# Kernel tuning notes

Hardware: AMD Instinct MI355X
Metric: run time of the kernel (lower is better)

The kernel has to match this reference:

```python
import jax, jax.numpy as jnp
import numpy as np


def setup_inputs() -> dict:
    key = jax.random.key(0)
    ks = jax.random.split(key, 7)
    T, D, V = 2048, 1024, 28  # frames, encoder hidden, vocab_size
    s = 0.05  # keras 'random_normal' initializer stddev
    return {
        "x": jax.random.normal(ks[0], (1, T, D), jnp.float32),
        "Wa": jax.random.normal(ks[1], (1, V), jnp.float32) * s,
        "Ua": jax.random.normal(ks[2], (1, D), jnp.float32) * s,
        "Va": jax.random.normal(ks[3], (1, 1), jnp.float32) * s,
        "Wo": jax.random.normal(ks[4], (V, V), jnp.float32) * s,
        "Uo": jax.random.normal(ks[5], (V, D), jnp.float32) * s,
        "Co": jax.random.normal(ks[6], (V, D), jnp.float32) * s,
    }


def reference(x, Wa, Ua, Va, Wo, Uo, Co):
    # Source uses only the first batch element: x = x[0]
    xb = x[0]                      # (T, D)
    V = Wo.shape[0]
    D = Uo.shape[1]
    # Ua . x[j] is constant across outer steps t (source recomputes it; math identical)
    ux = xb @ Ua[0]                # (T,)

    def step(carry, xt):
        Y, H = carry               # Y: (V,) previous output, H: (D,) previous frame
        prev = Wa[0] @ Y           # scalar: Wa . Yanterior
        scores = Va[0, 0] * jnp.tanh(ux + prev)   # (T,)
        # Source applies K.softmax (axis=-1) to scores of shape (T,1,1):
        # softmax over a size-1 axis -> all ones. Reproduced faithfully.
        w = jax.nn.softmax(scores[:, None], axis=-1)   # (T, 1), all ones
        context = (xb * w).sum(axis=0)                 # (D,)
        y = jax.nn.sigmoid(Wo @ Y + Uo @ H + Co @ context)  # (V,)
        return (y, xt), y          # Hanterior <- x[t]

    init = (jnp.zeros((V,), xb.dtype), jnp.zeros((D,), xb.dtype))
    _, ys = jax.lax.scan(step, init, xb)   # ys: (T, V)
    return ys[None]                        # (1, T, V)
```

## Files before the change

### kernel.cpp

```cpp
#include <hip/hip_runtime.h>

#define T_FRAMES 2048
#define D_DIM    1024
#define V_DIM    28
#define BSTRIDE  32
#define CSTRIDE  32
#define LOG2E_F  1.44269504088896f

#define CHUNK    8
#define WARM     24
#define NCHUNK   (T_FRAMES / CHUNK)

#define RPB      4
#define NB_PREP  (T_FRAMES / RPB)

__global__ __launch_bounds__(256) void prep_kernel(const float* __restrict__ x,
                                                   const float* __restrict__ Uo,
                                                   const float* __restrict__ Co,
                                                   float* __restrict__ cpart,
                                                   float* __restrict__ Bmat) {
    int tid = threadIdx.x, b = blockIdx.x;
    __shared__ float xs[RPB * D_DIM];
    __shared__ float cs[D_DIM];

    int wave = tid >> 6, lane = tid & 63;

    const float4* xb4 = (const float4*)(x + (size_t)b * RPB * D_DIM);
    float4 xv0 = xb4[0 * (D_DIM / 4) + tid];
    float4 xv1 = xb4[1 * (D_DIM / 4) + tid];
    float4 xv2 = xb4[2 * (D_DIM / 4) + tid];
    float4 xv3 = xb4[3 * (D_DIM / 4) + tid];

    float4 u[7][4];
#pragma unroll
    for (int q = 0; q < 7; ++q) {
        const float4* u4 = (const float4*)(Uo + (size_t)(wave * 7 + q) * D_DIM);
#pragma unroll
        for (int m = 0; m < 4; ++m) u[q][m] = u4[lane + 64 * m];
    }

    ((float4*)xs)[0 * (D_DIM / 4) + tid] = xv0;
    ((float4*)xs)[1 * (D_DIM / 4) + tid] = xv1;
    ((float4*)xs)[2 * (D_DIM / 4) + tid] = xv2;
    ((float4*)xs)[3 * (D_DIM / 4) + tid] = xv3;
    float4 csum;
    csum.x = (xv0.x + xv1.x) + (xv2.x + xv3.x);
    csum.y = (xv0.y + xv1.y) + (xv2.y + xv3.y);
    csum.z = (xv0.z + xv1.z) + (xv2.z + xv3.z);
    csum.w = (xv0.w + xv1.w) + (xv2.w + xv3.w);
    ((float4*)cs)[tid] = csum;
    __syncthreads();

#pragma unroll
    for (int q = 0; q < 7; ++q) {
        int i = wave * 7 + q;
        const float4* c4 = (const float4*)(Co + (size_t)i * D_DIM);
        float acc = 0.f;
#pragma unroll
        for (int m = 0; m < 4; ++m) {
            float4 a = c4[lane + 64 * m];
            float4 d = ((const float4*)cs)[lane + 64 * m];
            acc += a.x * d.x + a.y * d.y + a.z * d.z + a.w * d.w;
        }
#pragma unroll
        for (int off = 32; off > 0; off >>= 1) acc += __shfl_down(acc, off);
        if (lane == 0) cpart[(size_t)b * CSTRIDE + i] = acc;
    }
    if (tid == 0)
        *(float4*)(cpart + (size_t)b * CSTRIDE + V_DIM) = make_float4(0.f, 0.f, 0.f, 0.f);

#pragma unroll
    for (int r = 0; r < RPB; ++r) {
        int t = b * RPB + r + 1;
        if (t >= T_FRAMES) break;
        float4 xv[4];
#pragma unroll
        for (int m = 0; m < 4; ++m)
            xv[m] = ((const float4*)xs)[r * (D_DIM / 4) + lane + 64 * m];
#pragma unroll
        for (int q = 0; q < 7; ++q) {
            float acc = 0.f;
#pragma unroll
            for (int m = 0; m < 4; ++m) {
                acc = fmaf(u[q][m].x, xv[m].x, acc);
                acc = fmaf(u[q][m].y, xv[m].y, acc);
                acc = fmaf(u[q][m].z, xv[m].z, acc);
                acc = fmaf(u[q][m].w, xv[m].w, acc);
            }
#pragma unroll
            for (int off = 32; off > 0; off >>= 1) acc += __shfl_down(acc, off);
            if (lane == 0) Bmat[(size_t)t * BSTRIDE + wave * 7 + q] = acc * LOG2E_F;
        }
    }

    if (b == 0 && tid < BSTRIDE) Bmat[tid] = 0.f;
}

#define RL(j) __int_as_float(__builtin_amdgcn_readlane(yi_, j))

#define STEP(bval, ydst)                                                     \
    {                                                                        \
        int yi_ = __float_as_int(y);                                         \
        float a0 = (bval) + cik, a1 = 0.f, a2 = 0.f, a3 = 0.f;               \
        a0 = fmaf(w0,  RL(0),  a0);  a1 = fmaf(w1,  RL(1),  a1);             \
        a2 = fmaf(w2,  RL(2),  a2);  a3 = fmaf(w3,  RL(3),  a3);             \
        a0 = fmaf(w4,  RL(4),  a0);  a1 = fmaf(w5,  RL(5),  a1);             \
        a2 = fmaf(w6,  RL(6),  a2);  a3 = fmaf(w7,  RL(7),  a3);             \
        a0 = fmaf(w8,  RL(8),  a0);  a1 = fmaf(w9,  RL(9),  a1);             \
        a2 = fmaf(w10, RL(10), a2);  a3 = fmaf(w11, RL(11), a3);             \
        a0 = fmaf(w12, RL(12), a0);  a1 = fmaf(w13, RL(13), a1);             \
        a2 = fmaf(w14, RL(14), a2);  a3 = fmaf(w15, RL(15), a3);             \
        a0 = fmaf(w16, RL(16), a0);  a1 = fmaf(w17, RL(17), a1);             \
        a2 = fmaf(w18, RL(18), a2);  a3 = fmaf(w19, RL(19), a3);             \
        a0 = fmaf(w20, RL(20), a0);  a1 = fmaf(w21, RL(21), a1);             \
        a2 = fmaf(w22, RL(22), a2);  a3 = fmaf(w23, RL(23), a3);             \
        a0 = fmaf(w24, RL(24), a0);  a1 = fmaf(w25, RL(25), a1);             \
        a2 = fmaf(w26, RL(26), a2);  a3 = fmaf(w27, RL(27), a3);             \
        float acc_ = (a0 + a1) + (a2 + a3);                                  \
        y = __builtin_amdgcn_rcpf(1.f + __builtin_amdgcn_exp2f(-acc_));      \
        ydst = y;                                                            \
    }

#define SSTEP(n)                                                             \
    {                                                                        \
        int tn_ = (t + 1 < T_FRAMES) ? t + 1 : 0;                            \
        float bn_ = Bmat[(size_t)tn_ * BSTRIDE + bl];          \
        STEP(bcur, yb##n)                                                    \
        bcur = bn_; ++t;                                                     \
    }

__global__ __launch_bounds__(64, 1) void scan_kernel(const float* __restrict__ Bmat,
                                                     const float* __restrict__ cpart,
                                                     const float* __restrict__ Wo,
                                                     float* __restrict__ out) {
    int lane = threadIdx.x;
    bool act = lane < V_DIM;
    int bl   = lane & (BSTRIDE - 1);
    __shared__ float cfin[32];

    const float4* wrow = (const float4*)(Wo + (size_t)(act ? lane : 0) * V_DIM);
    float4 wqa = wrow[0], wqb = wrow[1], wqc = wrow[2], wqd = wrow[3];
    float4 wqe = wrow[4], wqf = wrow[5], wqg = wrow[6];

    int q8 = lane & 7;
    int bo = lane >> 3;
    const float4* cp4 = (const float4*)cpart;
    double d0 = 0.0, d1 = 0.0, d2 = 0.0, d3 = 0.0;
#pragma unroll
    for (int m = 0; m < NB_PREP / 8; ++m) {
        float4 v = cp4[(size_t)(m * 8 + bo) * (CSTRIDE / 4) + q8];
        d0 += v.x; d1 += v.y; d2 += v.z; d3 += v.w;
    }
#pragma unroll
    for (int off = 8; off < 64; off <<= 1) {
        d0 += __shfl_xor(d0, off);
        d1 += __shfl_xor(d1, off);
        d2 += __shfl_xor(d2, off);
        d3 += __shfl_xor(d3, off);
    }
    if (bo == 0) {
        cfin[q8 * 4 + 0] = (float)d0;
        cfin[q8 * 4 + 1] = (float)d1;
        cfin[q8 * 4 + 2] = (float)d2;
        cfin[q8 * 4 + 3] = (float)d3;
    }
    __syncthreads();
    float cik = cfin[lane & 31] * LOG2E_F;

    float w0  = wqa.x * LOG2E_F, w1  = wqa.y * LOG2E_F, w2  = wqa.z * LOG2E_F, w3  = wqa.w * LOG2E_F;
    float w4  = wqb.x * LOG2E_F, w5  = wqb.y * LOG2E_F, w6  = wqb.z * LOG2E_F, w7  = wqb.w * LOG2E_F;
    float w8  = wqc.x * LOG2E_F, w9  = wqc.y * LOG2E_F, w10 = wqc.z * LOG2E_F, w11 = wqc.w * LOG2E_F;
    float w12 = wqd.x * LOG2E_F, w13 = wqd.y * LOG2E_F, w14 = wqd.z * LOG2E_F, w15 = wqd.w * LOG2E_F;
    float w16 = wqe.x * LOG2E_F, w17 = wqe.y * LOG2E_F, w18 = wqe.z * LOG2E_F, w19 = wqe.w * LOG2E_F;
    float w20 = wqf.x * LOG2E_F, w21 = wqf.y * LOG2E_F, w22 = wqf.z * LOG2E_F, w23 = wqf.w * LOG2E_F;
    float w24 = wqg.x * LOG2E_F, w25 = wqg.y * LOG2E_F, w26 = wqg.z * LOG2E_F, w27 = wqg.w * LOG2E_F;

    int tstore = blockIdx.x * CHUNK;
    int t0     = tstore - WARM; if (t0 < 0) t0 = 0;
    int nwarm  = tstore - t0;

    float y    = 0.f;
    int   t    = t0;
    float bcur = Bmat[(size_t)t0 * BSTRIDE + bl];

    for (int s = 0; s < nwarm; ++s) {
        float bnext = Bmat[(size_t)(t + 1) * BSTRIDE + bl];
        float dump;
        STEP(bcur, dump)
        (void)dump;
        bcur = bnext; ++t;
    }

    float yb0, yb1, yb2, yb3, yb4, yb5, yb6, yb7;
    SSTEP(0) SSTEP(1) SSTEP(2) SSTEP(3)
    SSTEP(4) SSTEP(5) SSTEP(6) SSTEP(7)

    if (act) {
        float* op = out + (size_t)tstore * V_DIM + lane;
        op[0 * V_DIM] = yb0; op[1 * V_DIM] = yb1;
        op[2 * V_DIM] = yb2; op[3 * V_DIM] = yb3;
        op[4 * V_DIM] = yb4; op[5 * V_DIM] = yb5;
        op[6 * V_DIM] = yb6; op[7 * V_DIM] = yb7;
    }
}

extern "C" void kernel_launch(void* const* d_in, const int* in_sizes, int n_in,
                              void* d_out, int out_size, void* d_ws, size_t ws_size,
                              hipStream_t stream) {
    const float* x  = (const float*)d_in[0];
    const float* Wo = (const float*)d_in[4];
    const float* Uo = (const float*)d_in[5];
    const float* Co = (const float*)d_in[6];
    float* out = (float*)d_out;

    float* W     = (float*)d_ws;
    float* cpart = W;
    float* Bmat  = W + NB_PREP * CSTRIDE;

    prep_kernel<<<NB_PREP, 256, 0, stream>>>(x, Uo, Co, cpart, Bmat);
    scan_kernel<<<NCHUNK,  64,  0, stream>>>(Bmat, cpart, Wo, out);
}
```

Before: 94.64 us.

## Fuse prep and scan kernels into one cooperative launch with grid sync

The separate prep and scan kernels become one cooperative kernel of 256 blocks with 512 threads each. Every block first computes its share of the Co·context partials and the Uo·x B-matrix rows for 8 frames, then waits at a grid-wide sync, after which wave 0 runs the chunked scan. This removes a second kernel launch and the gap between launches. In exchange it pays for a cooperative launch and a grid barrier, and seven of the eight waves in each block sit idle during the scan.

```diff
diff --git a/kernel.cpp b/kernel.cpp
--- a/kernel.cpp
+++ b/kernel.cpp
@@ -1,4 +1,7 @@
 #include <hip/hip_runtime.h>
+#include <hip/hip_cooperative_groups.h>
+
+namespace cg = cooperative_groups;
 
 #define T_FRAMES 2048
 #define D_DIM    1024
@@ -9,92 +12,8 @@
 
 #define CHUNK    8
 #define WARM     24
-#define NCHUNK   (T_FRAMES / CHUNK)
-
-#define RPB      4
-#define NB_PREP  (T_FRAMES / RPB)
-
-__global__ __launch_bounds__(256) void prep_kernel(const float* __restrict__ x,
-                                                   const float* __restrict__ Uo,
-                                                   const float* __restrict__ Co,
-                                                   float* __restrict__ cpart,
-                                                   float* __restrict__ Bmat) {
-    int tid = threadIdx.x, b = blockIdx.x;
-    __shared__ float xs[RPB * D_DIM];
-    __shared__ float cs[D_DIM];
-
-    int wave = tid >> 6, lane = tid & 63;
-
-    const float4* xb4 = (const float4*)(x + (size_t)b * RPB * D_DIM);
-    float4 xv0 = xb4[0 * (D_DIM / 4) + tid];
-    float4 xv1 = xb4[1 * (D_DIM / 4) + tid];
-    float4 xv2 = xb4[2 * (D_DIM / 4) + tid];
-    float4 xv3 = xb4[3 * (D_DIM / 4) + tid];
-
-    float4 u[7][4];
-#pragma unroll
-    for (int q = 0; q < 7; ++q) {
-        const float4* u4 = (const float4*)(Uo + (size_t)(wave * 7 + q) * D_DIM);
-#pragma unroll
-        for (int m = 0; m < 4; ++m) u[q][m] = u4[lane + 64 * m];
-    }
-
-    ((float4*)xs)[0 * (D_DIM / 4) + tid] = xv0;
-    ((float4*)xs)[1 * (D_DIM / 4) + tid] = xv1;
-    ((float4*)xs)[2 * (D_DIM / 4) + tid] = xv2;
-    ((float4*)xs)[3 * (D_DIM / 4) + tid] = xv3;
-    float4 csum;
-    csum.x = (xv0.x + xv1.x) + (xv2.x + xv3.x);
-    csum.y = (xv0.y + xv1.y) + (xv2.y + xv3.y);
-    csum.z = (xv0.z + xv1.z) + (xv2.z + xv3.z);
-    csum.w = (xv0.w + xv1.w) + (xv2.w + xv3.w);
-    ((float4*)cs)[tid] = csum;
-    __syncthreads();
-
-#pragma unroll
-    for (int q = 0; q < 7; ++q) {
-        int i = wave * 7 + q;
-        const float4* c4 = (const float4*)(Co + (size_t)i * D_DIM);
-        float acc = 0.f;
-#pragma unroll
-        for (int m = 0; m < 4; ++m) {
-            float4 a = c4[lane + 64 * m];
-            float4 d = ((const float4*)cs)[lane + 64 * m];
-            acc += a.x * d.x + a.y * d.y + a.z * d.z + a.w * d.w;
-        }
-#pragma unroll
-        for (int off = 32; off > 0; off >>= 1) acc += __shfl_down(acc, off);
-        if (lane == 0) cpart[(size_t)b * CSTRIDE + i] = acc;
-    }
-    if (tid == 0)
-        *(float4*)(cpart + (size_t)b * CSTRIDE + V_DIM) = make_float4(0.f, 0.f, 0.f, 0.f);
-
-#pragma unroll
-    for (int r = 0; r < RPB; ++r) {
-        int t = b * RPB + r + 1;
-        if (t >= T_FRAMES) break;
-        float4 xv[4];
-#pragma unroll
-        for (int m = 0; m < 4; ++m)
-            xv[m] = ((const float4*)xs)[r * (D_DIM / 4) + lane + 64 * m];
-#pragma unroll
-        for (int q = 0; q < 7; ++q) {
-            float acc = 0.f;
-#pragma unroll
-            for (int m = 0; m < 4; ++m) {
-                acc = fmaf(u[q][m].x, xv[m].x, acc);
-                acc = fmaf(u[q][m].y, xv[m].y, acc);
-                acc = fmaf(u[q][m].z, xv[m].z, acc);
-                acc = fmaf(u[q][m].w, xv[m].w, acc);
-            }
-#pragma unroll
-            for (int off = 32; off > 0; off >>= 1) acc += __shfl_down(acc, off);
-            if (lane == 0) Bmat[(size_t)t * BSTRIDE + wave * 7 + q] = acc * LOG2E_F;
-        }
-    }
-
-    if (b == 0 && tid < BSTRIDE) Bmat[tid] = 0.f;
-}
+#define NBLK     256
+#define RPB      8
 
 #define RL(j) __int_as_float(__builtin_amdgcn_readlane(yi_, j))
 
@@ -129,25 +48,113 @@
         bcur = bn_; ++t;                                                     \
     }
 
-__global__ __launch_bounds__(64, 1) void scan_kernel(const float* __restrict__ Bmat,
-                                                     const float* __restrict__ cpart,
-                                                     const float* __restrict__ Wo,
-                                                     float* __restrict__ out) {
-    int lane = threadIdx.x;
-    bool act = lane < V_DIM;
-    int bl   = lane & (BSTRIDE - 1);
-    __shared__ float cfin[32];
-
-    const float4* wrow = (const float4*)(Wo + (size_t)(act ? lane : 0) * V_DIM);
-    float4 wqa = wrow[0], wqb = wrow[1], wqc = wrow[2], wqd = wrow[3];
-    float4 wqe = wrow[4], wqf = wrow[5], wqg = wrow[6];
-
-    int q8 = lane & 7;
-    int bo = lane >> 3;
+__global__ __launch_bounds__(512, 2) void fused_kernel(const float* __restrict__ x,
+                                                       const float* __restrict__ Uo,
+                                                       const float* __restrict__ Co,
+                                                       const float* __restrict__ Wo,
+                                                       float* __restrict__ cpart,
+                                                       float* __restrict__ Bmat,
+                                                       float* __restrict__ out) {
+    int tid = threadIdx.x, b = blockIdx.x;
+    int wave = tid >> 6, lane = tid & 63;
+    __shared__ float  xs[RPB * D_DIM];
+    __shared__ float4 cs2[512];
+    __shared__ float4 cs4[256];
+
+    float4 wqa, wqb, wqc, wqd, wqe, wqf, wqg;
+    if (wave == 0) {
+        const float4* wrow = (const float4*)(Wo + (size_t)((lane < V_DIM) ? lane : 0) * V_DIM);
+        wqa = wrow[0]; wqb = wrow[1]; wqc = wrow[2]; wqd = wrow[3];
+        wqe = wrow[4]; wqf = wrow[5]; wqg = wrow[6];
+    }
+
+    const float4* xb4 = (const float4*)(x + (size_t)b * (RPB * D_DIM));
+    float4 xl0 = xb4[tid], xl1 = xb4[tid + 512],
+           xl2 = xb4[tid + 1024], xl3 = xb4[tid + 1536];
+
+    int nr = (wave < 4) ? 4 : 3;
+    int r0 = (wave < 4) ? wave * 4 : 16 + (wave - 4) * 3;
+    float4 u[4][4];
+#pragma unroll
+    for (int q = 0; q < 4; ++q)
+        if (q < nr) {
+            const float4* u4 = (const float4*)(Uo + (size_t)(r0 + q) * D_DIM);
+#pragma unroll
+            for (int m = 0; m < 4; ++m) u[q][m] = u4[lane + 64 * m];
+        }
+
+    ((float4*)xs)[tid]        = xl0;
+    ((float4*)xs)[tid + 512]  = xl1;
+    ((float4*)xs)[tid + 1024] = xl2;
+    ((float4*)xs)[tid + 1536] = xl3;
+    float4 cp;
+    cp.x = (xl0.x + xl1.x) + (xl2.x + xl3.x);
+    cp.y = (xl0.y + xl1.y) + (xl2.y + xl3.y);
+    cp.z = (xl0.z + xl1.z) + (xl2.z + xl3.z);
+    cp.w = (xl0.w + xl1.w) + (xl2.w + xl3.w);
+    cs2[tid] = cp;
+    __syncthreads();
+    if (tid < 256) {
+        float4 a = cs2[tid], e = cs2[tid + 256];
+        cs4[tid] = make_float4(a.x + e.x, a.y + e.y, a.z + e.z, a.w + e.w);
+    }
+    if (b == 0 && tid < BSTRIDE) Bmat[tid] = 0.f;
+    __syncthreads();
+
+#pragma unroll
+    for (int q = 0; q < 4; ++q)
+        if (q < nr) {
+            int i = r0 + q;
+            const float4* c4 = (const float4*)(Co + (size_t)i * D_DIM);
+            float acc = 0.f;
+#pragma unroll
+            for (int m = 0; m < 4; ++m) {
+                float4 a = c4[lane + 64 * m];
+                float4 d = cs4[lane + 64 * m];
+                acc += a.x * d.x + a.y * d.y + a.z * d.z + a.w * d.w;
+            }
+#pragma unroll
+            for (int off = 32; off > 0; off >>= 1) acc += __shfl_down(acc, off);
+            if (lane == 0) cpart[(size_t)b * CSTRIDE + i] = acc;
+        }
+    if (tid == 0)
+        *(float4*)(cpart + (size_t)b * CSTRIDE + V_DIM) = make_float4(0.f, 0.f, 0.f, 0.f);
+
+#pragma unroll
+    for (int r = 0; r < RPB; ++r) {
+        int tt = b * RPB + r + 1;
+        if (tt < T_FRAMES) {
+            float4 xv[4];
+#pragma unroll
+            for (int m = 0; m < 4; ++m)
+                xv[m] = ((const float4*)xs)[r * 256 + lane + 64 * m];
+#pragma unroll
+            for (int q = 0; q < 4; ++q)
+                if (q < nr) {
+                    float acc = 0.f;
+#pragma unroll
+                    for (int m = 0; m < 4; ++m) {
+                        acc = fmaf(u[q][m].x, xv[m].x, acc);
+                        acc = fmaf(u[q][m].y, xv[m].y, acc);
+                        acc = fmaf(u[q][m].z, xv[m].z, acc);
+                        acc = fmaf(u[q][m].w, xv[m].w, acc);
+                    }
+#pragma unroll
+                    for (int off = 32; off > 0; off >>= 1) acc += __shfl_down(acc, off);
+                    if (lane == 0) Bmat[(size_t)tt * BSTRIDE + r0 + q] = acc * LOG2E_F;
+                }
+        }
+    }
+
+    cg::this_grid().sync();
+
+    if (wave != 0) return;
+
+    int q8 = lane & 7, bo = lane >> 3;
     const float4* cp4 = (const float4*)cpart;
     double d0 = 0.0, d1 = 0.0, d2 = 0.0, d3 = 0.0;
 #pragma unroll
-    for (int m = 0; m < NB_PREP / 8; ++m) {
+    for (int m = 0; m < NBLK / 8; ++m) {
         float4 v = cp4[(size_t)(m * 8 + bo) * (CSTRIDE / 4) + q8];
         d0 += v.x; d1 += v.y; d2 += v.z; d3 += v.w;
     }
@@ -158,14 +165,12 @@
         d2 += __shfl_xor(d2, off);
         d3 += __shfl_xor(d3, off);
     }
-    if (bo == 0) {
-        cfin[q8 * 4 + 0] = (float)d0;
-        cfin[q8 * 4 + 1] = (float)d1;
-        cfin[q8 * 4 + 2] = (float)d2;
-        cfin[q8 * 4 + 3] = (float)d3;
-    }
-    __syncthreads();
-    float cik = cfin[lane & 31] * LOG2E_F;
+    int src = lane >> 2;
+    double s0 = __shfl(d0, src), s1 = __shfl(d1, src);
+    double s2 = __shfl(d2, src), s3 = __shfl(d3, src);
+    int comp = lane & 3;
+    double cd = (comp == 0) ? s0 : (comp == 1) ? s1 : (comp == 2) ? s2 : s3;
+    float cik = (float)cd * LOG2E_F;
 
     float w0  = wqa.x * LOG2E_F, w1  = wqa.y * LOG2E_F, w2  = wqa.z * LOG2E_F, w3  = wqa.w * LOG2E_F;
     float w4  = wqb.x * LOG2E_F, w5  = wqb.y * LOG2E_F, w6  = wqb.z * LOG2E_F, w7  = wqb.w * LOG2E_F;
@@ -175,7 +180,8 @@
     float w20 = wqf.x * LOG2E_F, w21 = wqf.y * LOG2E_F, w22 = wqf.z * LOG2E_F, w23 = wqf.w * LOG2E_F;
     float w24 = wqg.x * LOG2E_F, w25 = wqg.y * LOG2E_F, w26 = wqg.z * LOG2E_F, w27 = wqg.w * LOG2E_F;
 
-    int tstore = blockIdx.x * CHUNK;
+    int bl     = lane & (BSTRIDE - 1);
+    int tstore = b * CHUNK;
     int t0     = tstore - WARM; if (t0 < 0) t0 = 0;
     int nwarm  = tstore - t0;
 
@@ -195,7 +201,7 @@
     SSTEP(0) SSTEP(1) SSTEP(2) SSTEP(3)
     SSTEP(4) SSTEP(5) SSTEP(6) SSTEP(7)
 
-    if (act) {
+    if (lane < V_DIM) {
         float* op = out + (size_t)tstore * V_DIM + lane;
         op[0 * V_DIM] = yb0; op[1 * V_DIM] = yb1;
         op[2 * V_DIM] = yb2; op[3 * V_DIM] = yb3;
@@ -215,8 +221,10 @@
 
     float* W     = (float*)d_ws;
     float* cpart = W;
-    float* Bmat  = W + NB_PREP * CSTRIDE;
-
-    prep_kernel<<<NB_PREP, 256, 0, stream>>>(x, Uo, Co, cpart, Bmat);
-    scan_kernel<<<NCHUNK,  64,  0, stream>>>(Bmat, cpart, Wo, out);
+    float* Bmat  = W + NBLK * CSTRIDE;
+
+    void* args[] = {(void*)&x, (void*)&Uo, (void*)&Co, (void*)&Wo,
+                    (void*)&cpart, (void*)&Bmat, (void*)&out};
+    hipLaunchCooperativeKernel((void*)fused_kernel, dim3(NBLK), dim3(512),
+                               args, 0, stream);
 }
```

Result: slower. 127.4 us (+34.6%).
